# Optimization experiments

Measured on AMD Instinct MI355X. Metric: run time of the kernel, lower is better.

Reference implementation:

```python
import jax, jax.numpy as jnp
import numpy as np
from jax import lax

U, K, POOL, STRIDE, FC = 300, 19, 7, 7, 100   # num_units, filter size, maxpool, fc_size
B, L, D = 256, 1000, 4                        # batch, seq len, DNA dim
P = (L - (K - 1) - (POOL - 1) - 1) // STRIDE + 1  # post_pool_size = 140
EPS = 1e-5  # BatchNorm eps (eval mode with running stats; Dropout is identity in eval)


def setup_inputs() -> dict:
    key = jax.random.key(0)
    ks = jax.random.split(key, 24)
    rn = lambda k, shp, s=0.1: jax.random.normal(k, shp, jnp.float32) * s
    return {
        "input_seq": jax.random.normal(ks[0], (B, L, D), jnp.float32),
        # per-unit conv (groups=U on tiled input == plain Conv1d(4, U, K))
        "w_conv": rn(ks[1], (U, D, K)), "b_conv": rn(ks[2], (U,)),
        "g1": 1.0 + rn(ks[3], (U,)), "be1": rn(ks[4], (U,)),
        "m1": rn(ks[5], (U,)), "v1": 1.0 + jax.random.uniform(ks[6], (U,), jnp.float32),
        # per-unit FC1 (grouped 1x1 conv: P -> FC per unit)
        "w_fc1": rn(ks[7], (U, FC, P)), "b_fc1": rn(ks[8], (U, FC)),
        "g2": 1.0 + rn(ks[9], (U, FC)), "be2": rn(ks[10], (U, FC)),
        "m2": rn(ks[11], (U, FC)), "v2": 1.0 + jax.random.uniform(ks[12], (U, FC), jnp.float32),
        # per-unit FC2 (grouped 1x1 conv: FC -> 1 per unit)
        "w_fc2": rn(ks[13], (U, FC)), "b_fc2": rn(ks[14], (U,)),
        "g3": 1.0 + rn(ks[15], (U,)), "be3": rn(ks[16], (U,)),
        "m3": rn(ks[17], (U,)), "v3": 1.0 + jax.random.uniform(ks[18], (U,), jnp.float32),
        # final Linear(U, 1)
        "w_out": rn(ks[19], (U, 1)), "b_out": rn(ks[20], (1,)),
    }


def reference(input_seq, w_conv, b_conv, g1, be1, m1, v1, w_fc1, b_fc1,
              g2, be2, m2, v2, w_fc2, b_fc2, g3, be3, m3, v3, w_out, b_out):
    x = jnp.transpose(input_seq, (0, 2, 1))  # B,D,L
    # grouped conv on input tiled U times: every group sees the same D=4 channels,
    # so it is exactly a plain Conv1d(D, U, K).
    conv = lax.conv_general_dilated(
        x, w_conv, (1,), 'VALID', dimension_numbers=('NCH', 'OIH', 'NCH')
    ) + b_conv[None, :, None]                 # B,U,L' (L'=L-K+1)
    a = (conv - m1[None, :, None]) * (g1 / jnp.sqrt(v1 + EPS))[None, :, None] + be1[None, :, None]
    a = jnp.exp(a)
    pooled = lax.reduce_window(a, -jnp.inf, lax.max,
                               (1, 1, POOL), (1, 1, STRIDE), 'VALID')  # B,U,P
    # Flatten->Unsqueeze->grouped 1x1 conv == per-unit matmul over P
    h = jnp.einsum('bup,ufp->buf', pooled, w_fc1) + b_fc1               # B,U,FC
    h = jax.nn.relu((h - m2) * (g2 / jnp.sqrt(v2 + EPS)) + be2)
    z = jnp.einsum('buf,uf->bu', h, w_fc2) + b_fc2                      # B,U
    z = jax.nn.relu((z - m3) * (g3 / jnp.sqrt(v3 + EPS)) + be3)
    return jax.nn.sigmoid(z @ w_out + b_out)                            # B,1
```

## Files before the change

kernel.cpp:

```cpp
#include <hip/hip_runtime.h>
#include <hip/hip_bf16.h>
#include <math.h>

#define U_   300
#define K_   19
#define FC_  100
#define B_   256
#define L_   1000
#define P_   140
#define EPS_ 1e-5f
#define WLD_ 144

typedef unsigned short ushort_t;
typedef __attribute__((ext_vector_type(8)))  short short8v;
typedef __attribute__((ext_vector_type(16))) float f32x16;

__device__ __forceinline__ ushort_t f2bf(float f) {
    union { float f; unsigned u; } a; a.f = f;
    unsigned r = a.u + 0x7fffu + ((a.u >> 16) & 1u);
    return (ushort_t)(r >> 16);
}

__global__ __launch_bounds__(256, 4)
void pack_conv_k(const float* __restrict__ w_conv, const float* __restrict__ b_conv,
                 const float* __restrict__ g1, const float* __restrict__ be1,
                 const float* __restrict__ m1, const float* __restrict__ v1,
                 ushort_t* __restrict__ w_bf, float* __restrict__ o1g)
{
    const int t = blockIdx.x * 256 + threadIdx.x;
    if (t < 320 * 80) {
        const int u = t / 80, j = t - u * 80;
        float val = 0.f;
        if (u < U_ && j < 76) {
            const int tp = j >> 2;
            const int d  = j & 3;
            const float s1 = g1[u] / sqrtf(v1[u] + EPS_);
            val = w_conv[u * 76 + 19 * d + tp] * s1;
        }
        const int nt = u >> 5, r = u & 31;
        const int kc = j >> 4, rem = j & 15;
        const int half = rem >> 3, e = rem & 7;
        w_bf[nt * 2560 + kc * 512 + half * 256 + r * 8 + e] = f2bf(val);
    }
    if (t < 320) {
        float o = 0.f;
        if (t < U_) {
            const float s1 = g1[t] / sqrtf(v1[t] + EPS_);
            o = (b_conv[t] - m1[t]) * s1 + be1[t];
        }
        o1g[t] = o;
    }
}

__global__ __launch_bounds__(448, 4)
void conv_mfma_k(const float4* __restrict__ x4,
                 const ushort_t* __restrict__ w_bf,
                 const float* __restrict__ o1g,
                 ushort_t* __restrict__ pooled)
{
    __shared__ ushort_t xls[880];
    __shared__ ushort_t wlds[25600];
    __shared__ float    o1l[320];
    __shared__ ushort_t stage[320][30];
    const int tid = threadIdx.x;
    const int bx  = blockIdx.x;
    const int b   = blockIdx.y;
    const int w0  = bx * 28;
    const int l0  = w0 * 7;

    if (tid < 220) {
        const int gi = l0 + tid;
        float4 v = make_float4(0.f, 0.f, 0.f, 0.f);
        if (gi < L_) v = x4[(size_t)b * L_ + gi];
        ushort4 pk4;
        pk4.x = f2bf(v.x); pk4.y = f2bf(v.y); pk4.z = f2bf(v.z); pk4.w = f2bf(v.w);
        *(ushort4*)&xls[4 * tid] = pk4;
    }
    {
        const float4* ws = (const float4*)w_bf;
        float4* wd = (float4*)wlds;
        for (int i = tid; i < 3200; i += 448) wd[i] = ws[i];
        if (tid < 320) o1l[tid] = o1g[tid];
    }
    __syncthreads();

    const int lane = tid & 63;
    const int mt   = tid >> 6;
    const int half = lane >> 5;
    const int r32  = lane & 31;

    const int sreg = (r32 & 3) + 4 * (r32 >> 3);
    const int sh   = (r32 >> 2) & 1;
    const int off  = sreg < 7  ? sreg + 7 * sh
                   : sreg < 14 ? sreg + 7 + 7 * sh
                               : 28 + (sreg - 14) + 2 * sh;

    const char* xb = (const char*)xls + 8 * (28 * mt + off) + 16 * half;
    const char* wl = (const char*)wlds + 16 * lane;

    short8v aA[5];
#pragma unroll
    for (int kc = 0; kc < 5; ++kc)
        aA[kc] = *(const short8v*)(xb + 32 * kc);

    const int pcol = 4 * mt + half;

#pragma unroll
    for (int nt = 0; nt < 10; ++nt) {
        short8v bfr[5];
#pragma unroll
        for (int kc = 0; kc < 5; ++kc)
            bfr[kc] = *(const short8v*)(wl + nt * 5120 + kc * 1024);
        const float o1u = o1l[nt * 32 + r32];

        f32x16 acc = {};
#pragma unroll
        for (int kc = 0; kc < 5; ++kc)
            acc = __builtin_amdgcn_mfma_f32_32x32x16_bf16(aA[kc], bfr[kc], acc, 0, 0, 0);

        float m0 = acc[0], m1 = acc[7];
#pragma unroll
        for (int j = 1; j < 7; ++j)  m0 = fmaxf(m0, acc[j]);
#pragma unroll
        for (int j = 8; j < 14; ++j) m1 = fmaxf(m1, acc[j]);

        stage[nt * 32 + r32][pcol]     = f2bf(__expf(m0 + o1u));
        stage[nt * 32 + r32][pcol + 2] = f2bf(__expf(m1 + o1u));
    }
    __syncthreads();

#pragma unroll
    for (int i = 0; i < 5; ++i) {
        const int idx = tid + 448 * i;
        const int row = idx / 7;
        const int cc  = idx - 7 * row;
        if (row < U_) {
            const ushort4 st = *(const ushort4*)&stage[row][4 * cc];
            *(ushort4*)&pooled[((size_t)row * B_ + b) * P_ + w0 + 4 * cc] = st;
        }
    }
}

__global__ __launch_bounds__(256, 3)
void fc_mfma_k(const ushort_t* __restrict__ pooled,
               const float* __restrict__ w_fc1,
               const float* __restrict__ b_fc1,
               const float* __restrict__ g2,
               const float* __restrict__ be2,
               const float* __restrict__ m2,
               const float* __restrict__ v2,
               const float* __restrict__ w_fc2,
               const float* __restrict__ b_fc2,
               const float* __restrict__ g3,
               const float* __restrict__ be3,
               const float* __restrict__ m3,
               const float* __restrict__ v3,
               float* __restrict__ zT)
{
    __shared__ ushort_t wlds[FC_ * WLD_];
    __shared__ float zred[128][33];
    const int tid  = threadIdx.x;
    const int bid = blockIdx.x;
    int u, bt;
    if (bid < 592) {
        const int r = bid & 7, k = bid >> 3;
        bt = k & 1;
        u  = (k >> 1) * 8 + r;
    } else {
        const int t = bid - 592;
        u  = 296 + (t >> 1);
        bt = t & 1;
    }

    const float* __restrict__ wsrc = w_fc1 + (size_t)u * FC_ * P_;
    for (int idx = tid; idx < FC_ * 35; idx += 256) {
        const int f = idx / 35, j = idx - f * 35;
        const float4 v = *(const float4*)(wsrc + f * P_ + 4 * j);
        ushort4 pk;
        pk.x = f2bf(v.x); pk.y = f2bf(v.y); pk.z = f2bf(v.z); pk.w = f2bf(v.w);
        *(ushort4*)&wlds[f * WLD_ + 4 * j] = pk;
    }
    for (int idx = tid; idx < FC_ * 4; idx += 256) {
        const int f = idx >> 2, k = 140 + (idx & 3);
        wlds[f * WLD_ + k] = 0;
    }
    __syncthreads();

    const int lane = tid & 63;
    const int wv   = tid >> 6;
    const int half = lane >> 5;
    const int r32  = lane & 31;

    const int brow = bt * 128 + wv * 32 + r32;
    const ushort_t* __restrict__ abase =
        pooled + ((size_t)u * B_ + brow) * P_ + half * 8;

    const ushort_t* __restrict__ bl0 = &wlds[r32 * WLD_ + half * 8];
    const ushort_t* __restrict__ bl1 = &wlds[(32 + r32) * WLD_ + half * 8];
    const ushort_t* __restrict__ bl2 = &wlds[(64 + r32) * WLD_ + half * 8];
    const int f3c = (96 + r32 < FC_) ? (96 + r32) : (FC_ - 1);
    const ushort_t* __restrict__ bl3 = &wlds[f3c * WLD_ + half * 8];

    short8v ac = *(const short8v*)(abase);
    f32x16 acc0 = {}, acc1 = {}, acc2 = {}, acc3 = {};
#pragma unroll
    for (int kc = 0; kc < 9; ++kc) {
        const int kn = (kc < 8) ? kc + 1 : kc;
        const short8v an = *(const short8v*)(abase + kn * 16);
        const short8v b0 = *(const short8v*)(bl0 + kc * 16);
        const short8v b1 = *(const short8v*)(bl1 + kc * 16);
        const short8v b2 = *(const short8v*)(bl2 + kc * 16);
        const short8v b3 = *(const short8v*)(bl3 + kc * 16);
        acc0 = __builtin_amdgcn_mfma_f32_32x32x16_bf16(ac, b0, acc0, 0, 0, 0);
        acc1 = __builtin_amdgcn_mfma_f32_32x32x16_bf16(ac, b1, acc1, 0, 0, 0);
        acc2 = __builtin_amdgcn_mfma_f32_32x32x16_bf16(ac, b2, acc2, 0, 0, 0);
        acc3 = __builtin_amdgcn_mfma_f32_32x32x16_bf16(ac, b3, acc3, 0, 0, 0);
        ac = an;
    }

    float s2[4], o2[4], w2[4];
#pragma unroll
    for (int n = 0; n < 4; ++n) {
        const int f = n * 32 + r32;
        if (f < FC_) {
            const int fg = u * FC_ + f;
            const float ss = g2[fg] / sqrtf(v2[fg] + EPS_);
            s2[n] = ss;
            o2[n] = (b_fc1[fg] - m2[fg]) * ss + be2[fg];
            w2[n] = w_fc2[fg];
        } else {
            s2[n] = 0.f; o2[n] = 0.f; w2[n] = 0.f;
        }
    }
#pragma unroll
    for (int rg = 0; rg < 16; ++rg) {
        const int row = (rg & 3) + 8 * (rg >> 2) + 4 * half;
        float s = fmaxf(fmaf(acc0[rg], s2[0], o2[0]), 0.f) * w2[0];
        s = fmaf(fmaxf(fmaf(acc1[rg], s2[1], o2[1]), 0.f), w2[1], s);
        s = fmaf(fmaxf(fmaf(acc2[rg], s2[2], o2[2]), 0.f), w2[2], s);
        s = fmaf(fmaxf(fmaf(acc3[rg], s2[3], o2[3]), 0.f), w2[3], s);
        zred[wv * 32 + row][r32] = s;
    }
    __syncthreads();

    if (tid < 128) {
        float s = 0.f;
#pragma unroll
        for (int j = 0; j < 32; ++j) s += zred[tid][j];
        const float s3 = g3[u] / sqrtf(v3[u] + EPS_);
        const float o3 = (b_fc2[u] - m3[u]) * s3 + be3[u];
        zT[(size_t)(bt * 128 + tid) * 304 + u] = fmaxf(fmaf(s, s3, o3), 0.f);
    }
}

__global__ __launch_bounds__(64, 8)
void out_k(const float* __restrict__ zT,
           const float* __restrict__ w_out,
           const float* __restrict__ b_out,
           float* __restrict__ out)
{
    const int lane = threadIdx.x;
    const int b    = blockIdx.x;
    const float4* zr = (const float4*)(zT + (size_t)b * 304);
    const float4* w4 = (const float4*)w_out;

    float s = 0.f;
    for (int i = lane; i < 75; i += 64) {
        const float4 z = zr[i], w = w4[i];
        s += z.x * w.x + z.y * w.y + z.z * w.z + z.w * w.w;
    }
#pragma unroll
    for (int o = 32; o > 0; o >>= 1) s += __shfl_xor(s, o);
    if (lane == 0)
        out[b] = 1.0f / (1.0f + __expf(-(s + b_out[0])));
}

extern "C" void kernel_launch(void* const* d_in, const int* in_sizes, int n_in,
                              void* d_out, int out_size, void* d_ws, size_t ws_size,
                              hipStream_t stream)
{
    const float* input_seq = (const float*)d_in[0];
    const float* w_conv    = (const float*)d_in[1];
    const float* b_conv    = (const float*)d_in[2];
    const float* g1        = (const float*)d_in[3];
    const float* be1       = (const float*)d_in[4];
    const float* m1        = (const float*)d_in[5];
    const float* v1        = (const float*)d_in[6];
    const float* w_fc1     = (const float*)d_in[7];
    const float* b_fc1     = (const float*)d_in[8];
    const float* g2        = (const float*)d_in[9];
    const float* be2       = (const float*)d_in[10];
    const float* m2        = (const float*)d_in[11];
    const float* v2        = (const float*)d_in[12];
    const float* w_fc2     = (const float*)d_in[13];
    const float* b_fc2     = (const float*)d_in[14];
    const float* g3        = (const float*)d_in[15];
    const float* be3       = (const float*)d_in[16];
    const float* m3        = (const float*)d_in[17];
    const float* v3        = (const float*)d_in[18];
    const float* w_out     = (const float*)d_in[19];
    const float* b_out     = (const float*)d_in[20];

    char* p = (char*)d_ws;
    ushort_t* pooled = (ushort_t*)p;   p += (size_t)B_ * U_ * P_ * 2;
    ushort_t* w_bf   = (ushort_t*)p;   p += 320 * 80 * 2;
    float*    o1g    = (float*)p;      p += 320 * 4;
    float*    zT     = (float*)p;      p += (size_t)B_ * 304 * 4;

    pack_conv_k<<<dim3(100), 256, 0, stream>>>(
        w_conv, b_conv, g1, be1, m1, v1, w_bf, o1g);

    conv_mfma_k<<<dim3(5, B_), 448, 0, stream>>>(
        (const float4*)input_seq, w_bf, o1g, pooled);

    fc_mfma_k<<<dim3(600), 256, 0, stream>>>(
        pooled, w_fc1, b_fc1, g2, be2, m2, v2, w_fc2, b_fc2,
        g3, be3, m3, v3, zT);

    out_k<<<dim3(B_), 64, 0, stream>>>(zT, w_out, b_out, (float*)d_out);
}
```

Measured before the change: 55.10 us.

## Retile conv kernel into smaller blocks reading weights from global, prefetch FC activations

The conv kernel now splits work over a 3D grid of 16-column windows and two halves of the unit range. It drops the per-block copy of all 50KB of bf16 weights into LDS and reads B fragments directly from global/L2, which lowers LDS use and raises occupancy. Output goes through a small per-tile stage buffer with two syncs per unit tile. Separately, the FC kernel issues all pooled A-fragment loads before the weight conversion, so global latency overlaps the LDS fill. In exchange, weight reads are repeated per block through cache, there are more barriers, and the A fragments cost more registers.

```diff
diff --git a/kernel.cpp b/kernel.cpp
--- a/kernel.cpp
+++ b/kernel.cpp
@@ -52,23 +52,22 @@
     }
 }
 
-__global__ __launch_bounds__(448, 4)
+__global__ __launch_bounds__(256, 6)
 void conv_mfma_k(const float4* __restrict__ x4,
                  const ushort_t* __restrict__ w_bf,
                  const float* __restrict__ o1g,
                  ushort_t* __restrict__ pooled)
 {
-    __shared__ ushort_t xls[880];
-    __shared__ ushort_t wlds[25600];
-    __shared__ float    o1l[320];
-    __shared__ ushort_t stage[320][30];
+    __shared__ ushort_t xls[544];
+    __shared__ ushort_t stage[32][18];
     const int tid = threadIdx.x;
     const int bx  = blockIdx.x;
-    const int b   = blockIdx.y;
-    const int w0  = bx * 28;
+    const int nh  = blockIdx.y;
+    const int b   = blockIdx.z;
+    const int w0  = bx * 16;
     const int l0  = w0 * 7;
 
-    if (tid < 220) {
+    if (tid < 136) {
         const int gi = l0 + tid;
         float4 v = make_float4(0.f, 0.f, 0.f, 0.f);
         if (gi < L_) v = x4[(size_t)b * L_ + gi];
@@ -76,16 +75,10 @@
         pk4.x = f2bf(v.x); pk4.y = f2bf(v.y); pk4.z = f2bf(v.z); pk4.w = f2bf(v.w);
         *(ushort4*)&xls[4 * tid] = pk4;
     }
-    {
-        const float4* ws = (const float4*)w_bf;
-        float4* wd = (float4*)wlds;
-        for (int i = tid; i < 3200; i += 448) wd[i] = ws[i];
-        if (tid < 320) o1l[tid] = o1g[tid];
-    }
     __syncthreads();
 
     const int lane = tid & 63;
-    const int mt   = tid >> 6;
+    const int wv   = tid >> 6;
     const int half = lane >> 5;
     const int r32  = lane & 31;
 
@@ -95,23 +88,24 @@
                    : sreg < 14 ? sreg + 7 + 7 * sh
                                : 28 + (sreg - 14) + 2 * sh;
 
-    const char* xb = (const char*)xls + 8 * (28 * mt + off) + 16 * half;
-    const char* wl = (const char*)wlds + 16 * lane;
+    const char* xb = (const char*)xls + 8 * (28 * wv + off) + 16 * half;
 
     short8v aA[5];
 #pragma unroll
     for (int kc = 0; kc < 5; ++kc)
         aA[kc] = *(const short8v*)(xb + 32 * kc);
 
-    const int pcol = 4 * mt + half;
-
-#pragma unroll
-    for (int nt = 0; nt < 10; ++nt) {
+    const char* wgl = (const char*)w_bf + nh * 5 * 5120 + 16 * lane;
+
+    const int p0off = 4 * wv + half;
+
+    for (int ntp = 0; ntp < 5; ++ntp) {
         short8v bfr[5];
 #pragma unroll
         for (int kc = 0; kc < 5; ++kc)
-            bfr[kc] = *(const short8v*)(wl + nt * 5120 + kc * 1024);
-        const float o1u = o1l[nt * 32 + r32];
+            bfr[kc] = *(const short8v*)(wgl + ntp * 5120 + kc * 1024);
+        const int ubase = nh * 160 + ntp * 32;
+        const float o1u = o1g[ubase + r32];
 
         f32x16 acc = {};
 #pragma unroll
@@ -124,20 +118,20 @@
 #pragma unroll
         for (int j = 8; j < 14; ++j) m1 = fmaxf(m1, acc[j]);
 
-        stage[nt * 32 + r32][pcol]     = f2bf(__expf(m0 + o1u));
-        stage[nt * 32 + r32][pcol + 2] = f2bf(__expf(m1 + o1u));
-    }
-    __syncthreads();
-
-#pragma unroll
-    for (int i = 0; i < 5; ++i) {
-        const int idx = tid + 448 * i;
-        const int row = idx / 7;
-        const int cc  = idx - 7 * row;
-        if (row < U_) {
-            const ushort4 st = *(const ushort4*)&stage[row][4 * cc];
-            *(ushort4*)&pooled[((size_t)row * B_ + b) * P_ + w0 + 4 * cc] = st;
+        stage[r32][p0off]     = f2bf(__expf(m0 + o1u));
+        stage[r32][p0off + 2] = f2bf(__expf(m1 + o1u));
+        __syncthreads();
+
+        if (tid < 128) {
+            const int du = tid >> 2, dc = tid & 3;
+            const int ug = ubase + du;
+            const int wq = w0 + 4 * dc;
+            if (ug < U_ && wq + 3 < P_) {
+                const ushort4 st = *(const ushort4*)&stage[du][4 * dc];
+                *(ushort4*)&pooled[((size_t)ug * B_ + b) * P_ + wq] = st;
+            }
         }
+        __syncthreads();
     }
 }
 
@@ -172,6 +166,19 @@
         bt = t & 1;
     }
 
+    const int lane = tid & 63;
+    const int wv   = tid >> 6;
+    const int half = lane >> 5;
+    const int r32  = lane & 31;
+
+    const int brow = bt * 128 + wv * 32 + r32;
+    const ushort_t* __restrict__ abase =
+        pooled + ((size_t)u * B_ + brow) * P_ + half * 8;
+    short8v a[9];
+#pragma unroll
+    for (int kc = 0; kc < 9; ++kc)
+        a[kc] = *(const short8v*)(abase + kc * 16);
+
     const float* __restrict__ wsrc = w_fc1 + (size_t)u * FC_ * P_;
     for (int idx = tid; idx < FC_ * 35; idx += 256) {
         const int f = idx / 35, j = idx - f * 35;
@@ -186,36 +193,23 @@
     }
     __syncthreads();
 
-    const int lane = tid & 63;
-    const int wv   = tid >> 6;
-    const int half = lane >> 5;
-    const int r32  = lane & 31;
-
-    const int brow = bt * 128 + wv * 32 + r32;
-    const ushort_t* __restrict__ abase =
-        pooled + ((size_t)u * B_ + brow) * P_ + half * 8;
-
     const ushort_t* __restrict__ bl0 = &wlds[r32 * WLD_ + half * 8];
     const ushort_t* __restrict__ bl1 = &wlds[(32 + r32) * WLD_ + half * 8];
     const ushort_t* __restrict__ bl2 = &wlds[(64 + r32) * WLD_ + half * 8];
     const int f3c = (96 + r32 < FC_) ? (96 + r32) : (FC_ - 1);
     const ushort_t* __restrict__ bl3 = &wlds[f3c * WLD_ + half * 8];
 
-    short8v ac = *(const short8v*)(abase);
     f32x16 acc0 = {}, acc1 = {}, acc2 = {}, acc3 = {};
 #pragma unroll
     for (int kc = 0; kc < 9; ++kc) {
-        const int kn = (kc < 8) ? kc + 1 : kc;
-        const short8v an = *(const short8v*)(abase + kn * 16);
         const short8v b0 = *(const short8v*)(bl0 + kc * 16);
         const short8v b1 = *(const short8v*)(bl1 + kc * 16);
         const short8v b2 = *(const short8v*)(bl2 + kc * 16);
         const short8v b3 = *(const short8v*)(bl3 + kc * 16);
-        acc0 = __builtin_amdgcn_mfma_f32_32x32x16_bf16(ac, b0, acc0, 0, 0, 0);
-        acc1 = __builtin_amdgcn_mfma_f32_32x32x16_bf16(ac, b1, acc1, 0, 0, 0);
-        acc2 = __builtin_amdgcn_mfma_f32_32x32x16_bf16(ac, b2, acc2, 0, 0, 0);
-        acc3 = __builtin_amdgcn_mfma_f32_32x32x16_bf16(ac, b3, acc3, 0, 0, 0);
-        ac = an;
+        acc0 = __builtin_amdgcn_mfma_f32_32x32x16_bf16(a[kc], b0, acc0, 0, 0, 0);
+        acc1 = __builtin_amdgcn_mfma_f32_32x32x16_bf16(a[kc], b1, acc1, 0, 0, 0);
+        acc2 = __builtin_amdgcn_mfma_f32_32x32x16_bf16(a[kc], b2, acc2, 0, 0, 0);
+        acc3 = __builtin_amdgcn_mfma_f32_32x32x16_bf16(a[kc], b3, acc3, 0, 0, 0);
     }
 
     float s2[4], o2[4], w2[4];
@@ -310,7 +304,7 @@
     pack_conv_k<<<dim3(100), 256, 0, stream>>>(
         w_conv, b_conv, g1, be1, m1, v1, w_bf, o1g);
 
-    conv_mfma_k<<<dim3(5, B_), 448, 0, stream>>>(
+    conv_mfma_k<<<dim3(9, 2, B_), 256, 0, stream>>>(
         (const float4*)input_seq, w_bf, o1g, pooled);
 
     fc_mfma_k<<<dim3(600), 256, 0, stream>>>(
```

Measured after the change: 53.25 us (median of 2 runs). -3.4%, faster.
